# Optimization experiments

Hardware: AMD Instinct MI355X
Metric: run time of the kernel (lower is better)

The kernel has to match this reference:

```python
import jax, jax.numpy as jnp
import numpy as np

EPS = 1e-5
B, L, DM, DI, DR, DS, K = 1, 1024, 2048, 4096, 128, 16, 3
DT_MAX, DT_MIN, DT_FLOOR = 0.1, 0.001, 1e-4


def setup_inputs() -> dict:
    key = jax.random.key(0)
    ks = jax.random.split(key, 10)
    sc = lambda k, sh, s=0.02: (jax.random.normal(k, sh, jnp.float32) * s)
    # dt_proj bias init (softplus-inverse of dt sampled log-uniform in [dt_min, dt_max])
    dt = jnp.exp(jax.random.uniform(ks[7], (DI,), jnp.float32)
                 * (np.log(DT_MAX) - np.log(DT_MIN)) + np.log(DT_MIN))
    dt = jnp.clip(dt, DT_FLOOR, None)
    inv_dt = dt + jnp.log(-jnp.expm1(-dt))
    dt_std = DR ** (-0.5)  # dt_rank**-0.5 * dt_scale
    return {
        "x": jax.random.normal(ks[0], (B, L, DM), jnp.float32),
        "h": jnp.zeros((B, L, DI, DS), jnp.float32),
        "norm_w": jnp.ones((DM,), jnp.float32),
        "in_proj_w": sc(ks[1], (2 * DI, DM)),
        "conv_w": sc(ks[2], (DI, 1, K), 0.1),      # depthwise: (out=DI, in/groups=1, K)
        "conv_b": jnp.zeros((DI,), jnp.float32),
        "x_proj_w": sc(ks[3], (DR + 2 * DS, DI)),
        "dt_proj_w": jax.random.uniform(ks[4], (DI, DR), jnp.float32, -dt_std, dt_std),
        "dt_proj_b": inv_dt,
        "A_log": jnp.log(jnp.tile(jnp.arange(1, DS + 1, dtype=jnp.float32), (DI, 1))),
        "D": jnp.ones((DI,), jnp.float32),
        "out_proj_w": sc(ks[5], (DM, DI)),
    }


def reference(x, h, norm_w, in_proj_w, conv_w, conv_b, x_proj_w,
              dt_proj_w, dt_proj_b, A_log, D, out_proj_w):
    # RMSNorm
    xn = x * jax.lax.rsqrt(jnp.mean(x * x, axis=-1, keepdims=True) + EPS) * norm_w
    # in_proj -> split into x-branch and gate z
    xz = xn @ in_proj_w.T                      # (B,L,2*DI)
    xs, z = xz[..., :DI], xz[..., DI:]
    # depthwise conv over sequence (padding preserves L for odd K)
    xc = jax.lax.conv_general_dilated(
        jnp.transpose(xs, (0, 2, 1)), conv_w, (1,), [((K - 1) // 2, (K - 1) // 2)],
        dimension_numbers=("NCH", "OIH", "NCH"), feature_group_count=DI)
    xc = jnp.transpose(xc, (0, 2, 1)) + conv_b  # (B,L,DI)
    xc = jax.nn.silu(xc)
    # ssm_step (elementwise over L; h is per-position state)
    A = -jnp.exp(A_log)                        # (DI,DS)
    dBC = xc @ x_proj_w.T                      # (B,L,DR+2*DS)
    delta = jax.nn.softplus(dBC[..., :DR] @ dt_proj_w.T + dt_proj_b)  # (B,L,DI)
    Bm = dBC[..., DR:DR + DS]                  # (B,L,DS)
    Cm = dBC[..., DR + DS:]                    # (B,L,DS)
    deltaA = jnp.exp(delta[..., None] * A)     # (B,L,DI,DS)
    BX = delta[..., None] * Bm[:, :, None, :] * xc[..., None]  # (B,L,DI,DS)
    h_new = deltaA * h + BX                    # (B,L,DI,DS)
    y = jnp.einsum("blds,bls->bld", h_new, Cm) + D * xc
    out = (y * jax.nn.silu(z)) @ out_proj_w.T + xn  # residual adds normed x
    return out, h_new
```

## Files before the change

### kernel.cpp

```cpp
#include <hip/hip_runtime.h>
#include <hip/hip_bf16.h>
#include <math.h>

#define L_   1024
#define DM_  2048
#define DI_  4096
#define DR_  128
#define DS_  16
#define DBC_ 160

typedef __attribute__((ext_vector_type(4))) float f32x4;
typedef __attribute__((ext_vector_type(8))) short s16x8;

__device__ inline unsigned short f2b(float f) {
  unsigned int u = __float_as_uint(f);
  u += 0x7fffu + ((u >> 16) & 1u);
  return (unsigned short)(u >> 16);
}
__device__ inline float b2f(unsigned short u) {
  return __uint_as_float(((unsigned int)u) << 16);
}

__device__ inline void gload_lds16(const void* g, void* l) {
  __builtin_amdgcn_global_load_lds(
      (const __attribute__((address_space(1))) void*)g,
      (__attribute__((address_space(3))) void*)l, 16, 0, 0);
}

__launch_bounds__(256)
__global__ void rms_convert_kernel(const float* __restrict__ x, const float* __restrict__ w,
                                   float* __restrict__ xn, unsigned short* __restrict__ xnb,
                                   const float* __restrict__ w_in, const float* __restrict__ w_out,
                                   const float* __restrict__ w_dt, const float* __restrict__ w_xp,
                                   unsigned short* __restrict__ wib, unsigned short* __restrict__ wob,
                                   unsigned short* __restrict__ dtwb, unsigned short* __restrict__ xpwb) {
  if (blockIdx.x < L_) {
    int l = blockIdx.x;
    const float4* xr = (const float4*)(x + (size_t)l * DM_);
    const float4* wr = (const float4*)w;
    float4 v0 = xr[threadIdx.x];
    float4 v1 = xr[threadIdx.x + 256];
    float ss = v0.x*v0.x + v0.y*v0.y + v0.z*v0.z + v0.w*v0.w
             + v1.x*v1.x + v1.y*v1.y + v1.z*v1.z + v1.w*v1.w;
    for (int off = 32; off > 0; off >>= 1) ss += __shfl_down(ss, off, 64);
    __shared__ float sbuf[4];
    int lane = threadIdx.x & 63, wid = threadIdx.x >> 6;
    if (lane == 0) sbuf[wid] = ss;
    __syncthreads();
    float tot = sbuf[0] + sbuf[1] + sbuf[2] + sbuf[3];
    float scale = rsqrtf(tot / (float)DM_ + 1e-5f);
    float4 w0 = wr[threadIdx.x], w1 = wr[threadIdx.x + 256];
    float4 o0, o1;
    o0.x = v0.x * scale * w0.x; o0.y = v0.y * scale * w0.y;
    o0.z = v0.z * scale * w0.z; o0.w = v0.w * scale * w0.w;
    o1.x = v1.x * scale * w1.x; o1.y = v1.y * scale * w1.y;
    o1.z = v1.z * scale * w1.z; o1.w = v1.w * scale * w1.w;
    float4* outr = (float4*)(xn + (size_t)l * DM_);
    outr[threadIdx.x] = o0;
    outr[threadIdx.x + 256] = o1;
    uint2 p0, p1;
    p0.x = (unsigned)f2b(o0.x) | ((unsigned)f2b(o0.y) << 16);
    p0.y = (unsigned)f2b(o0.z) | ((unsigned)f2b(o0.w) << 16);
    p1.x = (unsigned)f2b(o1.x) | ((unsigned)f2b(o1.y) << 16);
    p1.y = (unsigned)f2b(o1.z) | ((unsigned)f2b(o1.w) << 16);
    uint2* ob = (uint2*)(xnb + (size_t)l * DM_);
    ob[threadIdx.x] = p0;
    ob[threadIdx.x + 256] = p1;
    return;
  }
  const int N1 = 2 * DI_ * DM_ / 4;
  const int N2 = DM_ * DI_ / 4;
  const int N3 = DI_ * DR_ / 4;
  const int N4 = DBC_ * DI_ / 4;
  int i = (blockIdx.x - L_) * 256 + threadIdx.x;
  const float* src; unsigned short* dst; int off;
  if (i < N1)                { src = w_in;  dst = wib;  off = i; }
  else if (i < N1 + N2)      { src = w_out; dst = wob;  off = i - N1; }
  else if (i < N1 + N2 + N3) { src = w_dt;  dst = dtwb; off = i - N1 - N2; }
  else if (i < N1 + N2 + N3 + N4) { src = w_xp; dst = xpwb; off = i - N1 - N2 - N3; }
  else return;
  float4 v = ((const float4*)src)[off];
  uint2 p;
  p.x = (unsigned)f2b(v.x) | ((unsigned)f2b(v.y) << 16);
  p.y = (unsigned)f2b(v.z) | ((unsigned)f2b(v.w) << 16);
  ((uint2*)dst)[off] = p;
}

template<int EPI>
__launch_bounds__(256)
__global__ void gemm_bf16_mfma(const unsigned short* __restrict__ A,
                               const unsigned short* __restrict__ W,
                               void* __restrict__ Cv_, int M, int N, int K,
                               const float* __restrict__ aux) {
  __shared__ unsigned short As[128 * 32];
  __shared__ unsigned short Ws[128 * 32];
  int nwg = gridDim.x * gridDim.y;
  int flat = blockIdx.y * gridDim.x + blockIdx.x;
  int q8 = nwg >> 3;
  int swz = (flat & 7) * q8 + (flat >> 3);
  int bxi = swz % gridDim.x, byi = swz / gridDim.x;
  int bm = byi * 128, bn = bxi * 128;
  int tid = threadIdx.x;
  int w = tid >> 6, lane = tid & 63;
  int wr = (w >> 1) * 64, wc = (w & 1) * 64;
  f32x4 acc[4][4];
#pragma unroll
  for (int m = 0; m < 4; m++)
#pragma unroll
    for (int n = 0; n < 4; n++) acc[m][n] = (f32x4){0.f, 0.f, 0.f, 0.f};

  int kb = lane >> 4, r = lane & 15;
  for (int k0 = 0; k0 < K; k0 += 32) {
#pragma unroll
    for (int i = 0; i < 2; i++) {
      int ch = (i * 4 + w) * 64 + lane;
      int row = ch >> 2, kc = ch & 3;
      gload_lds16(A + (size_t)(bm + row) * K + k0 + kc * 8, As + ch * 8);
      gload_lds16(W + (size_t)(bn + row) * K + k0 + kc * 8, Ws + ch * 8);
    }
    asm volatile("s_waitcnt vmcnt(0)" ::: "memory");
    __syncthreads();
    s16x8 a[4], b[4];
#pragma unroll
    for (int m = 0; m < 4; m++)
      a[m] = *(const s16x8*)(As + (wr + m * 16 + r) * 32 + kb * 8);
#pragma unroll
    for (int n = 0; n < 4; n++)
      b[n] = *(const s16x8*)(Ws + (wc + n * 16 + r) * 32 + kb * 8);
#pragma unroll
    for (int m = 0; m < 4; m++)
#pragma unroll
      for (int n = 0; n < 4; n++)
        acc[m][n] = __builtin_amdgcn_mfma_f32_16x16x32_bf16(a[m], b[n], acc[m][n], 0, 0, 0);
    __syncthreads();
  }
  int q = lane >> 4;
#pragma unroll
  for (int m = 0; m < 4; m++) {
#pragma unroll
    for (int n = 0; n < 4; n++) {
#pragma unroll
      for (int j = 0; j < 4; j++) {
        int row = bm + wr + m * 16 + q * 4 + j;
        int col = bn + wc + n * 16 + r;
        float v = acc[m][n][j];
        if (EPI == 1) {
          v += aux[col];
          v = fmaxf(v, 0.f) + log1pf(__expf(-fabsf(v)));
          ((unsigned short*)Cv_)[(size_t)row * N + col] = f2b(v);
        }
        if (EPI == 3) {
          ((unsigned short*)Cv_)[(size_t)row * N + col] = f2b(v);
        }
      }
    }
  }
}

__launch_bounds__(256)
__global__ void gemm_bf16_mfma_bm64(const unsigned short* __restrict__ A,
                                    const unsigned short* __restrict__ W,
                                    float* __restrict__ C, int M, int N, int K,
                                    const float* __restrict__ aux) {
  __shared__ unsigned short As[64 * 32];
  __shared__ unsigned short Ws[128 * 32];
  int nwg = gridDim.x * gridDim.y;
  int flat = blockIdx.y * gridDim.x + blockIdx.x;
  int q8 = nwg >> 3;
  int swz = (flat & 7) * q8 + (flat >> 3);
  int bxi = swz % gridDim.x, byi = swz / gridDim.x;
  int bm = byi * 64, bn = bxi * 128;
  int tid = threadIdx.x;
  int w = tid >> 6, lane = tid & 63;
  int wr = (w >> 1) * 32, wc = (w & 1) * 64;
  f32x4 acc[2][4];
#pragma unroll
  for (int m = 0; m < 2; m++)
#pragma unroll
    for (int n = 0; n < 4; n++) acc[m][n] = (f32x4){0.f, 0.f, 0.f, 0.f};

  int kb = lane >> 4, r = lane & 15;
  for (int k0 = 0; k0 < K; k0 += 32) {
    {
      int ch = w * 64 + lane;
      int row = ch >> 2, kc = ch & 3;
      gload_lds16(A + (size_t)(bm + row) * K + k0 + kc * 8, As + ch * 8);
    }
#pragma unroll
    for (int i = 0; i < 2; i++) {
      int ch = (i * 4 + w) * 64 + lane;
      int row = ch >> 2, kc = ch & 3;
      gload_lds16(W + (size_t)(bn + row) * K + k0 + kc * 8, Ws + ch * 8);
    }
    asm volatile("s_waitcnt vmcnt(0)" ::: "memory");
    __syncthreads();
    s16x8 a[2], b[4];
#pragma unroll
    for (int m = 0; m < 2; m++)
      a[m] = *(const s16x8*)(As + (wr + m * 16 + r) * 32 + kb * 8);
#pragma unroll
    for (int n = 0; n < 4; n++)
      b[n] = *(const s16x8*)(Ws + (wc + n * 16 + r) * 32 + kb * 8);
#pragma unroll
    for (int m = 0; m < 2; m++)
#pragma unroll
      for (int n = 0; n < 4; n++)
        acc[m][n] = __builtin_amdgcn_mfma_f32_16x16x32_bf16(a[m], b[n], acc[m][n], 0, 0, 0);
    __syncthreads();
  }
  int q = lane >> 4;
#pragma unroll
  for (int m = 0; m < 2; m++) {
#pragma unroll
    for (int n = 0; n < 4; n++) {
#pragma unroll
      for (int j = 0; j < 4; j++) {
        int row = bm + wr + m * 16 + q * 4 + j;
        int col = bn + wc + n * 16 + r;
        C[(size_t)row * N + col] = acc[m][n][j] + aux[(size_t)row * N + col];
      }
    }
  }
}

__launch_bounds__(256)
__global__ void conv_silu_kernel(const unsigned short* __restrict__ xzb, const float* __restrict__ cw,
                                 const float* __restrict__ cb, unsigned short* __restrict__ xcb) {
  int idx = blockIdx.x * 256 + threadIdx.x;
  int l = idx >> 12, d = idx & (DI_ - 1);
  float w0 = cw[d * 3 + 0], w1 = cw[d * 3 + 1], w2 = cw[d * 3 + 2];
  float acc = cb[d];
  const unsigned short* base = xzb + d;
  if (l > 0)      acc = fmaf(w0, b2f(base[(size_t)(l - 1) * (2 * DI_)]), acc);
  acc = fmaf(w1, b2f(base[(size_t)l * (2 * DI_)]), acc);
  if (l < L_ - 1) acc = fmaf(w2, b2f(base[(size_t)(l + 1) * (2 * DI_)]), acc);
  float sig = 1.f / (1.f + __expf(-acc));
  xcb[idx] = f2b(acc * sig);
}

__launch_bounds__(256)
__global__ void xproj_stage1_mfma(const unsigned short* __restrict__ xcb,
                                  const unsigned short* __restrict__ Wb,
                                  float* __restrict__ part) {
  __shared__ unsigned short As[64 * 32];
  __shared__ unsigned short Bs[160 * 32];
  int sp = blockIdx.x;
  int l0 = blockIdx.y * 64;
  int tid = threadIdx.x, w = tid >> 6, lane = tid & 63;
  int wr = (w >> 1) * 32, wc = (w & 1) * 80;
  int kb = lane >> 4, r = lane & 15;
  f32x4 acc[2][5];
#pragma unroll
  for (int m = 0; m < 2; m++)
#pragma unroll
    for (int n = 0; n < 5; n++) acc[m][n] = (f32x4){0.f, 0.f, 0.f, 0.f};

  for (int kt = 0; kt < 8; kt++) {
    int k0 = sp * 256 + kt * 32;
    {
      int ch = w * 64 + lane;
      int row = ch >> 2, kc = ch & 3;
      gload_lds16(xcb + (size_t)(l0 + row) * DI_ + k0 + kc * 8, As + ch * 8);
    }
#pragma unroll
    for (int i = 0; i < 3; i++) {
      int g = i * 4 + w;
      if (g < 10) {
        int ch = g * 64 + lane;
        int row = ch >> 2, kc = ch & 3;
        gload_lds16(Wb + (size_t)row * DI_ + k0 + kc * 8, Bs + ch * 8);
      }
    }
    asm volatile("s_waitcnt vmcnt(0)" ::: "memory");
    __syncthreads();
    s16x8 a[2], b[5];
#pragma unroll
    for (int m = 0; m < 2; m++)
      a[m] = *(const s16x8*)(As + (wr + m * 16 + r) * 32 + kb * 8);
#pragma unroll
    for (int n = 0; n < 5; n++)
      b[n] = *(const s16x8*)(Bs + (wc + n * 16 + r) * 32 + kb * 8);
#pragma unroll
    for (int m = 0; m < 2; m++)
#pragma unroll
      for (int n = 0; n < 5; n++)
        acc[m][n] = __builtin_amdgcn_mfma_f32_16x16x32_bf16(a[m], b[n], acc[m][n], 0, 0, 0);
    __syncthreads();
  }
  int q = lane >> 4;
  float* pb = part + (size_t)sp * (L_ * DBC_) + (size_t)l0 * DBC_;
#pragma unroll
  for (int m = 0; m < 2; m++)
#pragma unroll
    for (int n = 0; n < 5; n++)
#pragma unroll
      for (int j = 0; j < 4; j++)
        pb[(size_t)(wr + m * 16 + q * 4 + j) * DBC_ + wc + n * 16 + r] = acc[m][n][j];
}

__launch_bounds__(256)
__global__ void xproj_stage2(const float* __restrict__ part, float* __restrict__ dBC,
                             unsigned short* __restrict__ dtb) {
  int i = blockIdx.x * 256 + threadIdx.x;
  float s = 0.f;
#pragma unroll
  for (int sp = 0; sp < 16; sp++) s += part[(size_t)sp * (L_ * DBC_) + i];
  dBC[i] = s;
  int l = i / DBC_, col = i - l * DBC_;
  if (col < DR_) dtb[(size_t)l * DR_ + col] = f2b(s);
}

__launch_bounds__(256)
__global__ void ssm_kernel2(const unsigned short* __restrict__ xzb, const unsigned short* __restrict__ xcb,
                            const float* __restrict__ dBC, const unsigned short* __restrict__ deltab,
                            const float* __restrict__ h, const float* __restrict__ A_log,
                            const float* __restrict__ Dp, float* __restrict__ h_out,
                            unsigned short* __restrict__ yzb) {
  int pair = threadIdx.x >> 2;
  int q = threadIdx.x & 3;
  for (int base = blockIdx.x * 64; base < L_ * DI_; base += gridDim.x * 64) {
    int idx = base + pair;
    int l = idx >> 12, d = idx & (DI_ - 1);
    float dv = b2f(deltab[idx]);
    float xv = b2f(xcb[idx]);
    float4 hv = *(const float4*)(h + (size_t)idx * DS_ + q * 4);
    float4 Al = *(const float4*)(A_log + (size_t)d * DS_ + q * 4);
    float4 Bv = *(const float4*)(dBC + (size_t)l * DBC_ + DR_ + q * 4);
    float4 Cv = *(const float4*)(dBC + (size_t)l * DBC_ + DR_ + DS_ + q * 4);
    float4 hn;
    hn.x = __expf(dv * -__expf(Al.x)) * hv.x + dv * Bv.x * xv;
    hn.y = __expf(dv * -__expf(Al.y)) * hv.y + dv * Bv.y * xv;
    hn.z = __expf(dv * -__expf(Al.z)) * hv.z + dv * Bv.z * xv;
    hn.w = __expf(dv * -__expf(Al.w)) * hv.w + dv * Bv.w * xv;
    *(float4*)(h_out + (size_t)idx * DS_ + q * 4) = hn;
    float y = hn.x * Cv.x + hn.y * Cv.y + hn.z * Cv.z + hn.w * Cv.w;
    y += __shfl_xor(y, 1, 64);
    y += __shfl_xor(y, 2, 64);
    if (q == 0) {
      y = fmaf(Dp[d], xv, y);
      float zv = b2f(xzb[(size_t)l * (2 * DI_) + DI_ + d]);
      float sig = 1.f / (1.f + __expf(-zv));
      yzb[idx] = f2b(y * zv * sig);
    }
  }
}

extern "C" void kernel_launch(void* const* d_in, const int* in_sizes, int n_in,
                              void* d_out, int out_size, void* d_ws, size_t ws_size,
                              hipStream_t stream) {
  const float* x         = (const float*)d_in[0];
  const float* h         = (const float*)d_in[1];
  const float* norm_w    = (const float*)d_in[2];
  const float* in_proj_w = (const float*)d_in[3];
  const float* conv_w    = (const float*)d_in[4];
  const float* conv_b    = (const float*)d_in[5];
  const float* x_proj_w  = (const float*)d_in[6];
  const float* dt_proj_w = (const float*)d_in[7];
  const float* dt_proj_b = (const float*)d_in[8];
  const float* A_log     = (const float*)d_in[9];
  const float* Dvec      = (const float*)d_in[10];
  const float* out_projw = (const float*)d_in[11];

  float* out   = (float*)d_out;
  float* h_out = out + (size_t)L_ * DM_;

  float* ws    = (float*)d_ws;
  float* xn    = ws;
  float* dBC   = xn    + (size_t)L_ * DM_;
  float* part  = dBC   + (size_t)L_ * DBC_;
  unsigned short* xnb   = (unsigned short*)(part + (size_t)16 * L_ * DBC_);
  unsigned short* wib   = xnb   + (size_t)L_ * DM_;
  unsigned short* wob   = wib   + (size_t)2 * DI_ * DM_;
  unsigned short* yzb   = wob   + (size_t)DM_ * DI_;
  unsigned short* dtb   = yzb   + (size_t)L_ * DI_;
  unsigned short* dtwb  = dtb   + (size_t)L_ * DR_;
  unsigned short* xpwb  = dtwb  + (size_t)DI_ * DR_;
  unsigned short* xcb   = xpwb  + (size_t)DBC_ * DI_;
  unsigned short* xzb   = xcb   + (size_t)L_ * DI_;
  unsigned short* deltab= xzb   + (size_t)L_ * 2 * DI_;

  const int CONV_BLKS = (2 * DI_ * DM_ + DM_ * DI_ + DI_ * DR_ + DBC_ * DI_) / 4 / 256;
  rms_convert_kernel<<<L_ + CONV_BLKS, 256, 0, stream>>>(
      x, norm_w, xn, xnb, in_proj_w, out_projw, dt_proj_w, x_proj_w, wib, wob, dtwb, xpwb);
  gemm_bf16_mfma<3><<<dim3(2 * DI_ / 128, L_ / 128), 256, 0, stream>>>(
      xnb, wib, xzb, L_, 2 * DI_, DM_, nullptr);
  conv_silu_kernel<<<L_ * DI_ / 256, 256, 0, stream>>>(xzb, conv_w, conv_b, xcb);
  xproj_stage1_mfma<<<dim3(16, 16), 256, 0, stream>>>(xcb, xpwb, part);
  xproj_stage2<<<L_ * DBC_ / 256, 256, 0, stream>>>(part, dBC, dtb);
  gemm_bf16_mfma<1><<<dim3(DI_ / 128, L_ / 128), 256, 0, stream>>>(
      dtb, dtwb, deltab, L_, DI_, DR_, dt_proj_b);
  ssm_kernel2<<<4096, 256, 0, stream>>>(
      xzb, xcb, dBC, deltab, h, A_log, Dvec, h_out, yzb);
  gemm_bf16_mfma_bm64<<<dim3(DM_ / 128, L_ / 64), 256, 0, stream>>>(
      yzb, wob, out, L_, DM_, DI_, xn);
}
```

Baseline: 330.7 us.

## Double-buffer LDS tiles in MFMA GEMM and x_proj kernels to overlap loads

Converts the three bf16 MFMA GEMM kernels (128x128, 64x128 and x_proj stage 1) to ping-pong LDS buffers. The next K-tile's global_load_lds is issued before computing on the current tile, so global-memory latency can overlap with the MFMA work. The explicit s_waitcnt vmcnt(0) before the barrier is removed, so correctness now relies on __syncthreads ordering the asynchronous LDS loads. LDS use doubles, which may lower occupancy.

```diff
diff --git a/kernel.cpp b/kernel.cpp
--- a/kernel.cpp
+++ b/kernel.cpp
@@ -92,8 +92,8 @@
                                const unsigned short* __restrict__ W,
                                void* __restrict__ Cv_, int M, int N, int K,
                                const float* __restrict__ aux) {
-  __shared__ unsigned short As[128 * 32];
-  __shared__ unsigned short Ws[128 * 32];
+  __shared__ unsigned short As[2][128 * 32];
+  __shared__ unsigned short Ws[2][128 * 32];
   int nwg = gridDim.x * gridDim.y;
   int flat = blockIdx.y * gridDim.x + blockIdx.x;
   int q8 = nwg >> 3;
@@ -103,6 +103,10 @@
   int tid = threadIdx.x;
   int w = tid >> 6, lane = tid & 63;
   int wr = (w >> 1) * 64, wc = (w & 1) * 64;
+  int ch0 = w * 64 + lane, ch1 = (4 + w) * 64 + lane;
+  int row0 = ch0 >> 2, kc0 = ch0 & 3;
+  int row1 = ch1 >> 2, kc1 = ch1 & 3;
+
   f32x4 acc[4][4];
 #pragma unroll
   for (int m = 0; m < 4; m++)
@@ -110,23 +114,28 @@
     for (int n = 0; n < 4; n++) acc[m][n] = (f32x4){0.f, 0.f, 0.f, 0.f};
 
   int kb = lane >> 4, r = lane & 15;
-  for (int k0 = 0; k0 < K; k0 += 32) {
-#pragma unroll
-    for (int i = 0; i < 2; i++) {
-      int ch = (i * 4 + w) * 64 + lane;
-      int row = ch >> 2, kc = ch & 3;
-      gload_lds16(A + (size_t)(bm + row) * K + k0 + kc * 8, As + ch * 8);
-      gload_lds16(W + (size_t)(bn + row) * K + k0 + kc * 8, Ws + ch * 8);
-    }
-    asm volatile("s_waitcnt vmcnt(0)" ::: "memory");
-    __syncthreads();
+
+#define STAGE_(buf, k0)                                                          \
+  do {                                                                           \
+    gload_lds16(A + (size_t)(bm + row0) * K + (k0) + kc0 * 8, &As[buf][ch0 * 8]);\
+    gload_lds16(W + (size_t)(bn + row0) * K + (k0) + kc0 * 8, &Ws[buf][ch0 * 8]);\
+    gload_lds16(A + (size_t)(bm + row1) * K + (k0) + kc1 * 8, &As[buf][ch1 * 8]);\
+    gload_lds16(W + (size_t)(bn + row1) * K + (k0) + kc1 * 8, &Ws[buf][ch1 * 8]);\
+  } while (0)
+
+  STAGE_(0, 0);
+  __syncthreads();
+  int nt = K >> 5;
+  for (int t = 0; t < nt; t++) {
+    int cur = t & 1;
+    if (t + 1 < nt) STAGE_(cur ^ 1, (t + 1) * 32);
     s16x8 a[4], b[4];
 #pragma unroll
     for (int m = 0; m < 4; m++)
-      a[m] = *(const s16x8*)(As + (wr + m * 16 + r) * 32 + kb * 8);
+      a[m] = *(const s16x8*)(&As[cur][(wr + m * 16 + r) * 32 + kb * 8]);
 #pragma unroll
     for (int n = 0; n < 4; n++)
-      b[n] = *(const s16x8*)(Ws + (wc + n * 16 + r) * 32 + kb * 8);
+      b[n] = *(const s16x8*)(&Ws[cur][(wc + n * 16 + r) * 32 + kb * 8]);
 #pragma unroll
     for (int m = 0; m < 4; m++)
 #pragma unroll
@@ -134,6 +143,7 @@
         acc[m][n] = __builtin_amdgcn_mfma_f32_16x16x32_bf16(a[m], b[n], acc[m][n], 0, 0, 0);
     __syncthreads();
   }
+#undef STAGE_
   int q = lane >> 4;
 #pragma unroll
   for (int m = 0; m < 4; m++) {
@@ -162,8 +172,8 @@
                                     const unsigned short* __restrict__ W,
                                     float* __restrict__ C, int M, int N, int K,
                                     const float* __restrict__ aux) {
-  __shared__ unsigned short As[64 * 32];
-  __shared__ unsigned short Ws[128 * 32];
+  __shared__ unsigned short As[2][64 * 32];
+  __shared__ unsigned short Ws[2][128 * 32];
   int nwg = gridDim.x * gridDim.y;
   int flat = blockIdx.y * gridDim.x + blockIdx.x;
   int q8 = nwg >> 3;
@@ -173,6 +183,11 @@
   int tid = threadIdx.x;
   int w = tid >> 6, lane = tid & 63;
   int wr = (w >> 1) * 32, wc = (w & 1) * 64;
+  int chA = w * 64 + lane;
+  int rowA = chA >> 2, kcA = chA & 3;
+  int ch0 = w * 64 + lane, ch1 = (4 + w) * 64 + lane;
+  int row0 = ch0 >> 2, kc0 = ch0 & 3;
+  int row1 = ch1 >> 2, kc1 = ch1 & 3;
   f32x4 acc[2][4];
 #pragma unroll
   for (int m = 0; m < 2; m++)
@@ -180,27 +195,27 @@
     for (int n = 0; n < 4; n++) acc[m][n] = (f32x4){0.f, 0.f, 0.f, 0.f};
 
   int kb = lane >> 4, r = lane & 15;
-  for (int k0 = 0; k0 < K; k0 += 32) {
-    {
-      int ch = w * 64 + lane;
-      int row = ch >> 2, kc = ch & 3;
-      gload_lds16(A + (size_t)(bm + row) * K + k0 + kc * 8, As + ch * 8);
-    }
-#pragma unroll
-    for (int i = 0; i < 2; i++) {
-      int ch = (i * 4 + w) * 64 + lane;
-      int row = ch >> 2, kc = ch & 3;
-      gload_lds16(W + (size_t)(bn + row) * K + k0 + kc * 8, Ws + ch * 8);
-    }
-    asm volatile("s_waitcnt vmcnt(0)" ::: "memory");
-    __syncthreads();
+
+#define STAGE_(buf, k0)                                                          \
+  do {                                                                           \
+    gload_lds16(A + (size_t)(bm + rowA) * K + (k0) + kcA * 8, &As[buf][chA * 8]);\
+    gload_lds16(W + (size_t)(bn + row0) * K + (k0) + kc0 * 8, &Ws[buf][ch0 * 8]);\
+    gload_lds16(W + (size_t)(bn + row1) * K + (k0) + kc1 * 8, &Ws[buf][ch1 * 8]);\
+  } while (0)
+
+  STAGE_(0, 0);
+  __syncthreads();
+  int nt = K >> 5;
+  for (int t = 0; t < nt; t++) {
+    int cur = t & 1;
+    if (t + 1 < nt) STAGE_(cur ^ 1, (t + 1) * 32);
     s16x8 a[2], b[4];
 #pragma unroll
     for (int m = 0; m < 2; m++)
-      a[m] = *(const s16x8*)(As + (wr + m * 16 + r) * 32 + kb * 8);
+      a[m] = *(const s16x8*)(&As[cur][(wr + m * 16 + r) * 32 + kb * 8]);
 #pragma unroll
     for (int n = 0; n < 4; n++)
-      b[n] = *(const s16x8*)(Ws + (wc + n * 16 + r) * 32 + kb * 8);
+      b[n] = *(const s16x8*)(&Ws[cur][(wc + n * 16 + r) * 32 + kb * 8]);
 #pragma unroll
     for (int m = 0; m < 2; m++)
 #pragma unroll
@@ -208,6 +223,7 @@
         acc[m][n] = __builtin_amdgcn_mfma_f32_16x16x32_bf16(a[m], b[n], acc[m][n], 0, 0, 0);
     __syncthreads();
   }
+#undef STAGE_
   int q = lane >> 4;
 #pragma unroll
   for (int m = 0; m < 2; m++) {
@@ -242,44 +258,48 @@
 __global__ void xproj_stage1_mfma(const unsigned short* __restrict__ xcb,
                                   const unsigned short* __restrict__ Wb,
                                   float* __restrict__ part) {
-  __shared__ unsigned short As[64 * 32];
-  __shared__ unsigned short Bs[160 * 32];
+  __shared__ unsigned short As[2][64 * 32];
+  __shared__ unsigned short Bs[2][160 * 32];
   int sp = blockIdx.x;
   int l0 = blockIdx.y * 64;
   int tid = threadIdx.x, w = tid >> 6, lane = tid & 63;
   int wr = (w >> 1) * 32, wc = (w & 1) * 80;
   int kb = lane >> 4, r = lane & 15;
+  int chA = w * 64 + lane;
+  int rowA = chA >> 2, kcA = chA & 3;
   f32x4 acc[2][5];
 #pragma unroll
   for (int m = 0; m < 2; m++)
 #pragma unroll
     for (int n = 0; n < 5; n++) acc[m][n] = (f32x4){0.f, 0.f, 0.f, 0.f};
 
+#define STAGE_(buf, k0)                                                            \
+  do {                                                                             \
+    gload_lds16(xcb + (size_t)(l0 + rowA) * DI_ + (k0) + kcA * 8, &As[buf][chA * 8]);\
+    _Pragma("unroll")                                                              \
+    for (int i = 0; i < 3; i++) {                                                  \
+      int g = i * 4 + w;                                                           \
+      if (g < 10) {                                                                \
+        int ch = g * 64 + lane;                                                    \
+        int row = ch >> 2, kc = ch & 3;                                            \
+        gload_lds16(Wb + (size_t)row * DI_ + (k0) + kc * 8, &Bs[buf][ch * 8]);     \
+      }                                                                            \
+    }                                                                              \
+  } while (0)
+
+  int kbase = sp * 256;
+  STAGE_(0, kbase);
+  __syncthreads();
   for (int kt = 0; kt < 8; kt++) {
-    int k0 = sp * 256 + kt * 32;
-    {
-      int ch = w * 64 + lane;
-      int row = ch >> 2, kc = ch & 3;
-      gload_lds16(xcb + (size_t)(l0 + row) * DI_ + k0 + kc * 8, As + ch * 8);
-    }
-#pragma unroll
-    for (int i = 0; i < 3; i++) {
-      int g = i * 4 + w;
-      if (g < 10) {
-        int ch = g * 64 + lane;
-        int row = ch >> 2, kc = ch & 3;
-        gload_lds16(Wb + (size_t)row * DI_ + k0 + kc * 8, Bs + ch * 8);
-      }
-    }
-    asm volatile("s_waitcnt vmcnt(0)" ::: "memory");
-    __syncthreads();
+    int cur = kt & 1;
+    if (kt + 1 < 8) STAGE_(cur ^ 1, kbase + (kt + 1) * 32);
     s16x8 a[2], b[5];
 #pragma unroll
     for (int m = 0; m < 2; m++)
-      a[m] = *(const s16x8*)(As + (wr + m * 16 + r) * 32 + kb * 8);
+      a[m] = *(const s16x8*)(&As[cur][(wr + m * 16 + r) * 32 + kb * 8]);
 #pragma unroll
     for (int n = 0; n < 5; n++)
-      b[n] = *(const s16x8*)(Bs + (wc + n * 16 + r) * 32 + kb * 8);
+      b[n] = *(const s16x8*)(&Bs[cur][(wc + n * 16 + r) * 32 + kb * 8]);
 #pragma unroll
     for (int m = 0; m < 2; m++)
 #pragma unroll
@@ -287,6 +307,7 @@
         acc[m][n] = __builtin_amdgcn_mfma_f32_16x16x32_bf16(a[m], b[n], acc[m][n], 0, 0, 0);
     __syncthreads();
   }
+#undef STAGE_
   int q = lane >> 4;
   float* pb = part + (size_t)sp * (L_ * DBC_) + (size_t)l0 * DBC_;
 #pragma unroll
```

Result: faster. 322.4 us (-2.5%).
